# Kernel tuning notes

Measured on AMD Instinct MI355X. Metric: run time of the kernel, lower is better.

The kernel has to match this reference:

```python
import jax, jax.numpy as jnp
import numpy as np

EPS = 1e-8
LN_EPS = 1e-5

def _layernorm(x, g, b):
    mu = jnp.mean(x, axis=-1, keepdims=True)
    var = jnp.mean((x - mu) ** 2, axis=-1, keepdims=True)
    return (x - mu) / jnp.sqrt(var + LN_EPS) * g + b

def setup_inputs() -> dict:
    key = jax.random.key(0)
    ks = jax.random.split(key, 10)
    B, S = 8192, 4096
    input_dim, hidden_dim = 4, 256
    h4 = hidden_dim // 4  # 64
    price_series = jax.random.uniform(ks[0], (B, S, 1), dtype=jnp.float32) + 0.5
    # 4 parallel encoders stacked on leading axis: Linear(input_dim->h4) + LayerNorm(h4)
    enc_w = jax.random.normal(ks[1], (4, input_dim, h4), dtype=jnp.float32) * 0.5
    enc_b = jax.random.normal(ks[2], (4, h4), dtype=jnp.float32) * 0.02
    enc_g = jnp.ones((4, h4), dtype=jnp.float32)
    enc_beta = jnp.zeros((4, h4), dtype=jnp.float32)
    # regime head: Linear(hidden_dim->64) + ReLU + (Dropout eval=identity) + Linear(64->4)
    head_w1 = jax.random.normal(ks[3], (hidden_dim, 64), dtype=jnp.float32) * 0.0625
    head_b1 = jnp.zeros((64,), dtype=jnp.float32)
    head_w2 = jax.random.normal(ks[4], (64, 4), dtype=jnp.float32) * 0.125
    head_b2 = jnp.zeros((4,), dtype=jnp.float32)
    return {"price_series": price_series, "enc_w": enc_w, "enc_b": enc_b,
            "enc_g": enc_g, "enc_beta": enc_beta,
            "head_w1": head_w1, "head_b1": head_b1,
            "head_w2": head_w2, "head_b2": head_b2}

def reference(price_series, enc_w, enc_b, enc_g, enc_beta, head_w1, head_b1, head_w2, head_b2):
    prices = price_series[:, :, 0]  # [B, S]
    B, S = prices.shape
    # Rolling SMA(20) with clamped window start, via cumsum (single pass, no per-step loop)
    csum = jnp.concatenate([jnp.zeros((B, 1), prices.dtype), jnp.cumsum(prices, axis=1)], axis=1)  # [B, S+1]
    i = jnp.arange(S)
    start20 = jnp.maximum(0, i - 19)
    cnt20 = (i - start20 + 1).astype(prices.dtype)
    sma20 = (csum[:, i + 1] - csum[:, start20]) / cnt20  # [B, S]
    trend_signal = (prices - sma20) / (sma20 + EPS)
    f_trend = jnp.mean(trend_signal, axis=1, keepdims=True)  # [B,1]
    # momentum over last 10 steps
    p_last = prices[:, -1:]
    p_m10 = prices[:, -10:-9]
    f_mom = (p_last - p_m10) / (p_m10 + EPS)  # [B,1]
    # mean reversion
    p_mean = jnp.mean(prices, axis=1, keepdims=True)
    f_mr = (p_last - p_mean) / (p_mean + EPS)  # [B,1]
    # cycle: coefficient of variation (torch.std is unbiased, ddof=1)
    f_cyc = jnp.std(prices, axis=1, ddof=1, keepdims=True) / (p_mean + EPS)  # [B,1]
    combined = jnp.concatenate([f_trend, f_mom, f_mr, f_cyc], axis=1)  # [B, 4]
    # 4 parallel encoders: Linear -> ReLU -> LayerNorm
    pre = jnp.einsum('bi,eio->ebo', combined, enc_w) + enc_b[:, None, :]  # [4, B, 64]
    feats = _layernorm(jax.nn.relu(pre), enc_g[:, None, :], enc_beta[:, None, :])  # [4, B, 64]
    # concat order: trend, momentum, mean_rev, cycle along feature dim
    regime_features = jnp.transpose(feats, (1, 0, 2)).reshape(B, -1)  # [B, 256]
    h = jax.nn.relu(regime_features @ head_w1 + head_b1)
    regime_probs = jax.nn.softmax(h @ head_w2 + head_b2, axis=1)  # [B, 4]
    return (regime_features, regime_probs)
```

## Files before the change

kernel.cpp:

```cpp
#include <hip/hip_runtime.h>

#define EPS 1e-8f
#define LN_EPS 1e-5f
#define NROWS 8192
#define SLEN 4096
#define PROBS_OFF 2097152

typedef __attribute__((ext_vector_type(8))) short bf16x8;
typedef __attribute__((ext_vector_type(4))) float f32x4;

__device__ __forceinline__ short f2bf(float f) {
    unsigned u = __float_as_uint(f);
    unsigned r = (u + 0x7FFFu + ((u >> 16) & 1u)) >> 16;
    return (short)r;
}

__global__ __launch_bounds__(256) void k_features(const float* __restrict__ prices,
                                                  float* __restrict__ out) {
    __shared__ float s[SLEN];
    __shared__ float red[12];
    const int b = blockIdx.x;
    const int t = threadIdx.x;
    const float* rowp = prices + (size_t)b * SLEN;

    #pragma unroll
    for (int i = 0; i < 4; ++i) {
        int idx = (i * 256 + t) * 4;
        float4 v = *(const float4*)(rowp + idx);
        *(float4*)(s + idx) = v;
    }
    __syncthreads();

    const int p0 = t * 16;
    float seg[16], prev[20];
    #pragma unroll
    for (int i = 0; i < 4; ++i)
        *(float4*)(seg + 4*i) = *(const float4*)(s + p0 + 4*i);
    #pragma unroll
    for (int i = 0; i < 5; ++i) {
        int base = p0 - 20 + 4*i;
        float4 pv;
        if (base >= 0) pv = *(const float4*)(s + base);
        else pv = make_float4(0.f, 0.f, 0.f, 0.f);
        *(float4*)(prev + 4*i) = pv;
    }

    float W = seg[0];
    #pragma unroll
    for (int j = 1; j < 20; ++j) W += prev[j];

    float x = seg[0];
    float sum = x, sq = x * x;
    float cnt = fminf((float)(p0 + 1), 20.0f);
    float sma = W * __builtin_amdgcn_rcpf(cnt);
    float ts = (x - sma) * __builtin_amdgcn_rcpf(sma + EPS);
    #pragma unroll
    for (int j = 1; j < 16; ++j) {
        x = seg[j];
        W += x - prev[j];
        sum += x;
        sq = fmaf(x, x, sq);
        float c2 = fminf((float)(p0 + j + 1), 20.0f);
        float sm = W * __builtin_amdgcn_rcpf(c2);
        ts += (x - sm) * __builtin_amdgcn_rcpf(sm + EPS);
    }

    #pragma unroll
    for (int off = 32; off > 0; off >>= 1) {
        sum += __shfl_xor(sum, off);
        sq  += __shfl_xor(sq,  off);
        ts  += __shfl_xor(ts,  off);
    }
    const int wv = t >> 6, lane = t & 63;
    if (lane == 0) { red[wv*3] = sum; red[wv*3+1] = sq; red[wv*3+2] = ts; }
    __syncthreads();

    if (t == 0) {
        float S = red[0] + red[3] + red[6] + red[9];
        float Q = red[1] + red[4] + red[7] + red[10];
        float T = red[2] + red[5] + red[8] + red[11];
        float mean = S * (1.0f / 4096.0f);
        float var  = fmaxf((Q - 4096.0f * mean * mean) * (1.0f / 4095.0f), 0.0f);
        float p_last = s[SLEN - 1];
        float p_m10  = s[SLEN - 10];
        float4 c;
        c.x = T * (1.0f / 4096.0f);
        c.y = (p_last - p_m10) / (p_m10 + EPS);
        c.z = (p_last - mean) / (mean + EPS);
        c.w = sqrtf(var) / (mean + EPS);
        *(float4*)(out + (size_t)b * 256) = c;
    }
}

#define ROWS 32

__global__ __launch_bounds__(256) void k_head(
    float* __restrict__ out,
    const float* __restrict__ enc_w, const float* __restrict__ enc_b,
    const float* __restrict__ enc_g, const float* __restrict__ enc_bt,
    const float* __restrict__ w1, const float* __restrict__ b1,
    const float* __restrict__ w2, const float* __restrict__ b2)
{
    __shared__ float comb[ROWS][4];
    __shared__ short rfb[ROWS][264];
    __shared__ float hbuf[ROWS][68];

    const int t = threadIdx.x;
    const int r0 = blockIdx.x * ROWS;
    const int lane = t & 63, wave = t >> 6;
    const int l15 = lane & 15, q = lane >> 4;

    if (t < ROWS * 4)
        comb[t >> 2][t & 3] = out[(size_t)(r0 + (t >> 2)) * 256 + (t & 3)];

    bf16x8 bfrag[8];
    #pragma unroll
    for (int kt = 0; kt < 8; ++kt) {
        #pragma unroll
        for (int j = 0; j < 8; ++j) {
            int k = kt * 32 + q * 8 + j;
            bfrag[kt][j] = f2bf(w1[k * 64 + wave * 16 + l15]);
        }
    }

    const float ew0 = enc_w[wave * 256 + lane];
    const float ew1v = enc_w[wave * 256 + 64 + lane];
    const float ew2v = enc_w[wave * 256 + 128 + lane];
    const float ew3v = enc_w[wave * 256 + 192 + lane];
    const float ebv = enc_b[t], egv = enc_g[t], btv = enc_bt[t];

    __syncthreads();

    for (int r = 0; r < ROWS; ++r) {
        float4 cb = *(const float4*)comb[r];
        float v = fmaf(cb.x, ew0, fmaf(cb.y, ew1v, fmaf(cb.z, ew2v, fmaf(cb.w, ew3v, ebv))));
        v = fmaxf(v, 0.0f);
        float sm = v;
        #pragma unroll
        for (int off = 32; off > 0; off >>= 1) sm += __shfl_xor(sm, off);
        float mu = sm * (1.0f / 64.0f);
        float d = v - mu;
        float vs = d * d;
        #pragma unroll
        for (int off = 32; off > 0; off >>= 1) vs += __shfl_xor(vs, off);
        float y = fmaf(d * rsqrtf(vs * (1.0f / 64.0f) + LN_EPS), egv, btv);
        out[(size_t)(r0 + r) * 256 + t] = y;
        rfb[r][t] = f2bf(y);
    }
    __syncthreads();

    f32x4 acc0 = {0.f, 0.f, 0.f, 0.f}, acc1 = {0.f, 0.f, 0.f, 0.f};
    #pragma unroll
    for (int kt = 0; kt < 8; ++kt) {
        bf16x8 a0 = *(const bf16x8*)&rfb[l15][kt * 32 + q * 8];
        bf16x8 a1 = *(const bf16x8*)&rfb[16 + l15][kt * 32 + q * 8];
        acc0 = __builtin_amdgcn_mfma_f32_16x16x32_bf16(a0, bfrag[kt], acc0, 0, 0, 0);
        acc1 = __builtin_amdgcn_mfma_f32_16x16x32_bf16(a1, bfrag[kt], acc1, 0, 0, 0);
    }

    const int col = wave * 16 + l15;
    const float b1v = b1[col];
    #pragma unroll
    for (int rg = 0; rg < 4; ++rg) {
        hbuf[q * 4 + rg][col]      = fmaxf(acc0[rg] + b1v, 0.0f);
        hbuf[16 + q * 4 + rg][col] = fmaxf(acc1[rg] + b1v, 0.0f);
    }
    __syncthreads();

    if (t < 128) {
        int r = t >> 2, c = t & 3;
        float lg = b2[c];
        #pragma unroll
        for (int j = 0; j < 64; ++j) lg = fmaf(hbuf[r][j], w2[j * 4 + c], lg);
        float mx = fmaxf(lg, __shfl_xor(lg, 1, 4));
        mx = fmaxf(mx, __shfl_xor(mx, 2, 4));
        float ex = __expf(lg - mx);
        float s2 = ex + __shfl_xor(ex, 1, 4);
        s2 += __shfl_xor(s2, 2, 4);
        out[PROBS_OFF + (size_t)(r0 + r) * 4 + c] = ex / s2;
    }
}

extern "C" void kernel_launch(void* const* d_in, const int* in_sizes, int n_in,
                              void* d_out, int out_size, void* d_ws, size_t ws_size,
                              hipStream_t stream) {
    const float* prices  = (const float*)d_in[0];
    const float* enc_w   = (const float*)d_in[1];
    const float* enc_b   = (const float*)d_in[2];
    const float* enc_g   = (const float*)d_in[3];
    const float* enc_bt  = (const float*)d_in[4];
    const float* head_w1 = (const float*)d_in[5];
    const float* head_b1 = (const float*)d_in[6];
    const float* head_w2 = (const float*)d_in[7];
    const float* head_b2 = (const float*)d_in[8];
    float* out = (float*)d_out;

    k_features<<<NROWS, 256, 0, stream>>>(prices, out);
    k_head<<<NROWS / ROWS, 256, 0, stream>>>(out, enc_w, enc_b, enc_g, enc_bt,
                                             head_w1, head_b1, head_w2, head_b2);
}
```

Measured before the change: 223.6 us.

## Fuse feature extraction and regime head into one per-row kernel

Merges the statistics kernel and the encoder/MLP head kernel into a single kernel with one block per row. The head is computed in fp32 FMA loops instead of bf16 MFMA, and the features read prices straight from global memory instead of staging the row in LDS. This removes a launch, the round-trip of the combined features through global memory, and the LDS staging, but every block now rereads the 64 KB head_w1 and does scalar matvec work, which could add cache traffic and ALU time to a kernel that is memory-bound.

```diff
diff --git a/kernel.cpp b/kernel.cpp
--- a/kernel.cpp
+++ b/kernel.cpp
@@ -6,43 +6,36 @@
 #define SLEN 4096
 #define PROBS_OFF 2097152
 
-typedef __attribute__((ext_vector_type(8))) short bf16x8;
-typedef __attribute__((ext_vector_type(4))) float f32x4;
+__global__ __launch_bounds__(256) void k_fused(
+    const float* __restrict__ prices,
+    const float* __restrict__ enc_w, const float* __restrict__ enc_b,
+    const float* __restrict__ enc_g, const float* __restrict__ enc_bt,
+    const float* __restrict__ w1, const float* __restrict__ b1,
+    const float* __restrict__ w2, const float* __restrict__ b2,
+    float* __restrict__ out)
+{
+    __shared__ float red[16];
+    __shared__ float tailv[2];
+    __shared__ float rfl[256];
+    __shared__ float hpart[4][64];
 
-__device__ __forceinline__ short f2bf(float f) {
-    unsigned u = __float_as_uint(f);
-    unsigned r = (u + 0x7FFFu + ((u >> 16) & 1u)) >> 16;
-    return (short)r;
-}
+    const int t = threadIdx.x;
+    const int b = blockIdx.x;
+    const int lane = t & 63, wv = t >> 6;
+    const float* rowp = prices + (size_t)b * SLEN;
+    const int p0 = t * 16;
 
-__global__ __launch_bounds__(256) void k_features(const float* __restrict__ prices,
-                                                  float* __restrict__ out) {
-    __shared__ float s[SLEN];
-    __shared__ float red[12];
-    const int b = blockIdx.x;
-    const int t = threadIdx.x;
-    const float* rowp = prices + (size_t)b * SLEN;
-
-    #pragma unroll
-    for (int i = 0; i < 4; ++i) {
-        int idx = (i * 256 + t) * 4;
-        float4 v = *(const float4*)(rowp + idx);
-        *(float4*)(s + idx) = v;
-    }
-    __syncthreads();
-
-    const int p0 = t * 16;
     float seg[16], prev[20];
     #pragma unroll
     for (int i = 0; i < 4; ++i)
-        *(float4*)(seg + 4*i) = *(const float4*)(s + p0 + 4*i);
+        *(float4*)(seg + 4 * i) = *(const float4*)(rowp + p0 + 4 * i);
     #pragma unroll
     for (int i = 0; i < 5; ++i) {
-        int base = p0 - 20 + 4*i;
+        int base = p0 - 20 + 4 * i;
         float4 pv;
-        if (base >= 0) pv = *(const float4*)(s + base);
+        if (base >= 0) pv = *(const float4*)(rowp + base);
         else pv = make_float4(0.f, 0.f, 0.f, 0.f);
-        *(float4*)(prev + 4*i) = pv;
+        *(float4*)(prev + 4 * i) = pv;
     }
 
     float W = seg[0];
@@ -71,113 +64,71 @@
         sq  += __shfl_xor(sq,  off);
         ts  += __shfl_xor(ts,  off);
     }
-    const int wv = t >> 6, lane = t & 63;
-    if (lane == 0) { red[wv*3] = sum; red[wv*3+1] = sq; red[wv*3+2] = ts; }
+    if (lane == 0) { red[wv * 4] = sum; red[wv * 4 + 1] = sq; red[wv * 4 + 2] = ts; }
+    if (t == 255) { tailv[0] = seg[15]; tailv[1] = seg[6]; }
     __syncthreads();
 
-    if (t == 0) {
-        float S = red[0] + red[3] + red[6] + red[9];
-        float Q = red[1] + red[4] + red[7] + red[10];
-        float T = red[2] + red[5] + red[8] + red[11];
-        float mean = S * (1.0f / 4096.0f);
-        float var  = fmaxf((Q - 4096.0f * mean * mean) * (1.0f / 4095.0f), 0.0f);
-        float p_last = s[SLEN - 1];
-        float p_m10  = s[SLEN - 10];
-        float4 c;
-        c.x = T * (1.0f / 4096.0f);
-        c.y = (p_last - p_m10) / (p_m10 + EPS);
-        c.z = (p_last - mean) / (mean + EPS);
-        c.w = sqrtf(var) / (mean + EPS);
-        *(float4*)(out + (size_t)b * 256) = c;
-    }
-}
+    float S = red[0] + red[4] + red[8]  + red[12];
+    float Q = red[1] + red[5] + red[9]  + red[13];
+    float T = red[2] + red[6] + red[10] + red[14];
+    float mean = S * (1.0f / 4096.0f);
+    float var  = fmaxf((Q - 4096.0f * mean * mean) * (1.0f / 4095.0f), 0.0f);
+    float p_last = tailv[0], p_m10 = tailv[1];
+    float c0 = T * (1.0f / 4096.0f);
+    float c1 = (p_last - p_m10) / (p_m10 + EPS);
+    float c2f = (p_last - mean) / (mean + EPS);
+    float c3 = sqrtf(var) / (mean + EPS);
 
-#define ROWS 32
-
-__global__ __launch_bounds__(256) void k_head(
-    float* __restrict__ out,
-    const float* __restrict__ enc_w, const float* __restrict__ enc_b,
-    const float* __restrict__ enc_g, const float* __restrict__ enc_bt,
-    const float* __restrict__ w1, const float* __restrict__ b1,
-    const float* __restrict__ w2, const float* __restrict__ b2)
-{
-    __shared__ float comb[ROWS][4];
-    __shared__ short rfb[ROWS][264];
-    __shared__ float hbuf[ROWS][68];
-
-    const int t = threadIdx.x;
-    const int r0 = blockIdx.x * ROWS;
-    const int lane = t & 63, wave = t >> 6;
-    const int l15 = lane & 15, q = lane >> 4;
-
-    if (t < ROWS * 4)
-        comb[t >> 2][t & 3] = out[(size_t)(r0 + (t >> 2)) * 256 + (t & 3)];
-
-    bf16x8 bfrag[8];
+    float v = enc_b[t];
+    v = fmaf(c0, enc_w[wv * 256 + lane],       v);
+    v = fmaf(c1, enc_w[wv * 256 + 64 + lane],  v);
+    v = fmaf(c2f, enc_w[wv * 256 + 128 + lane], v);
+    v = fmaf(c3, enc_w[wv * 256 + 192 + lane], v);
+    v = fmaxf(v, 0.0f);
+    float sm = v;
     #pragma unroll
-    for (int kt = 0; kt < 8; ++kt) {
-        #pragma unroll
-        for (int j = 0; j < 8; ++j) {
-            int k = kt * 32 + q * 8 + j;
-            bfrag[kt][j] = f2bf(w1[k * 64 + wave * 16 + l15]);
-        }
-    }
-
-    const float ew0 = enc_w[wave * 256 + lane];
-    const float ew1v = enc_w[wave * 256 + 64 + lane];
-    const float ew2v = enc_w[wave * 256 + 128 + lane];
-    const float ew3v = enc_w[wave * 256 + 192 + lane];
-    const float ebv = enc_b[t], egv = enc_g[t], btv = enc_bt[t];
-
+    for (int off = 32; off > 0; off >>= 1) sm += __shfl_xor(sm, off);
+    float mu = sm * (1.0f / 64.0f);
+    float d = v - mu;
+    float vs = d * d;
+    #pragma unroll
+    for (int off = 32; off > 0; off >>= 1) vs += __shfl_xor(vs, off);
+    float y = fmaf(d * rsqrtf(vs * (1.0f / 64.0f) + LN_EPS), enc_g[t], enc_bt[t]);
+    out[(size_t)b * 256 + t] = y;
+    rfl[t] = y;
     __syncthreads();
 
-    for (int r = 0; r < ROWS; ++r) {
-        float4 cb = *(const float4*)comb[r];
-        float v = fmaf(cb.x, ew0, fmaf(cb.y, ew1v, fmaf(cb.z, ew2v, fmaf(cb.w, ew3v, ebv))));
-        v = fmaxf(v, 0.0f);
-        float sm = v;
-        #pragma unroll
-        for (int off = 32; off > 0; off >>= 1) sm += __shfl_xor(sm, off);
-        float mu = sm * (1.0f / 64.0f);
-        float d = v - mu;
-        float vs = d * d;
-        #pragma unroll
-        for (int off = 32; off > 0; off >>= 1) vs += __shfl_xor(vs, off);
-        float y = fmaf(d * rsqrtf(vs * (1.0f / 64.0f) + LN_EPS), egv, btv);
-        out[(size_t)(r0 + r) * 256 + t] = y;
-        rfb[r][t] = f2bf(y);
+    {
+        float acc = 0.0f;
+        const float* w1p = w1 + (size_t)(wv * 64) * 64 + lane;
+        #pragma unroll 8
+        for (int k = 0; k < 64; ++k)
+            acc = fmaf(rfl[wv * 64 + k], w1p[k * 64], acc);
+        hpart[wv][lane] = acc;
     }
     __syncthreads();
 
-    f32x4 acc0 = {0.f, 0.f, 0.f, 0.f}, acc1 = {0.f, 0.f, 0.f, 0.f};
-    #pragma unroll
-    for (int kt = 0; kt < 8; ++kt) {
-        bf16x8 a0 = *(const bf16x8*)&rfb[l15][kt * 32 + q * 8];
-        bf16x8 a1 = *(const bf16x8*)&rfb[16 + l15][kt * 32 + q * 8];
-        acc0 = __builtin_amdgcn_mfma_f32_16x16x32_bf16(a0, bfrag[kt], acc0, 0, 0, 0);
-        acc1 = __builtin_amdgcn_mfma_f32_16x16x32_bf16(a1, bfrag[kt], acc1, 0, 0, 0);
-    }
-
-    const int col = wave * 16 + l15;
-    const float b1v = b1[col];
-    #pragma unroll
-    for (int rg = 0; rg < 4; ++rg) {
-        hbuf[q * 4 + rg][col]      = fmaxf(acc0[rg] + b1v, 0.0f);
-        hbuf[16 + q * 4 + rg][col] = fmaxf(acc1[rg] + b1v, 0.0f);
-    }
-    __syncthreads();
-
-    if (t < 128) {
-        int r = t >> 2, c = t & 3;
-        float lg = b2[c];
+    if (t < 64) {
+        float h = hpart[0][t] + hpart[1][t] + hpart[2][t] + hpart[3][t] + b1[t];
+        h = fmaxf(h, 0.0f);
+        float4 wrow = *(const float4*)(w2 + t * 4);
+        float l0 = h * wrow.x, l1 = h * wrow.y, l2 = h * wrow.z, l3 = h * wrow.w;
         #pragma unroll
-        for (int j = 0; j < 64; ++j) lg = fmaf(hbuf[r][j], w2[j * 4 + c], lg);
-        float mx = fmaxf(lg, __shfl_xor(lg, 1, 4));
-        mx = fmaxf(mx, __shfl_xor(mx, 2, 4));
-        float ex = __expf(lg - mx);
-        float s2 = ex + __shfl_xor(ex, 1, 4);
-        s2 += __shfl_xor(s2, 2, 4);
-        out[PROBS_OFF + (size_t)(r0 + r) * 4 + c] = ex / s2;
+        for (int off = 32; off > 0; off >>= 1) {
+            l0 += __shfl_xor(l0, off);
+            l1 += __shfl_xor(l1, off);
+            l2 += __shfl_xor(l2, off);
+            l3 += __shfl_xor(l3, off);
+        }
+        if (t == 0) {
+            l0 += b2[0]; l1 += b2[1]; l2 += b2[2]; l3 += b2[3];
+            float mx = fmaxf(fmaxf(l0, l1), fmaxf(l2, l3));
+            float e0 = __expf(l0 - mx), e1 = __expf(l1 - mx);
+            float e2 = __expf(l2 - mx), e3 = __expf(l3 - mx);
+            float inv = 1.0f / (e0 + e1 + e2 + e3);
+            float4 pr = make_float4(e0 * inv, e1 * inv, e2 * inv, e3 * inv);
+            *(float4*)(out + PROBS_OFF + (size_t)b * 4) = pr;
+        }
     }
 }
 
@@ -195,7 +146,6 @@
     const float* head_b2 = (const float*)d_in[8];
     float* out = (float*)d_out;
 
-    k_features<<<NROWS, 256, 0, stream>>>(prices, out);
-    k_head<<<NROWS / ROWS, 256, 0, stream>>>(out, enc_w, enc_b, enc_g, enc_bt,
-                                             head_w1, head_b1, head_w2, head_b2);
+    k_fused<<<NROWS, 256, 0, stream>>>(prices, enc_w, enc_b, enc_g, enc_bt,
+                                       head_w1, head_b1, head_w2, head_b2, out);
 }
```

Result: slower. 228.4 us (+2.1%).

## Process one price row per wavefront with direct global loads, no LDS

Applied to the files above, without the earlier changes.

The feature kernel now gives each 64-lane wavefront a whole row, and each lane handles 64 consecutive elements loaded straight from global memory instead of staging the row in shared memory. The block-level reduction and syncthreads go away, leaving only a wave shuffle reduction. The combined features are written to a workspace buffer rather than the output. Per-lane loads are now strided by 256 bytes across lanes, which hurts coalescing. The register count also grows (a 64-float segment per lane), which may lower occupancy on a memory-bound kernel.

```diff
diff --git a/kernel.cpp b/kernel.cpp
--- a/kernel.cpp
+++ b/kernel.cpp
@@ -15,34 +15,25 @@
     return (short)r;
 }
 
-__global__ __launch_bounds__(256) void k_features(const float* __restrict__ prices,
-                                                  float* __restrict__ out) {
-    __shared__ float s[SLEN];
-    __shared__ float red[12];
-    const int b = blockIdx.x;
+__global__ __launch_bounds__(256) void k_feat(const float* __restrict__ prices,
+                                              float* __restrict__ comb) {
     const int t = threadIdx.x;
+    const int lane = t & 63, wv = t >> 6;
+    const int b = blockIdx.x * 4 + wv;
     const float* rowp = prices + (size_t)b * SLEN;
+    const int p0 = lane * 64;
 
+    float seg[64], prev[20];
     #pragma unroll
-    for (int i = 0; i < 4; ++i) {
-        int idx = (i * 256 + t) * 4;
-        float4 v = *(const float4*)(rowp + idx);
-        *(float4*)(s + idx) = v;
-    }
-    __syncthreads();
-
-    const int p0 = t * 16;
-    float seg[16], prev[20];
-    #pragma unroll
-    for (int i = 0; i < 4; ++i)
-        *(float4*)(seg + 4*i) = *(const float4*)(s + p0 + 4*i);
+    for (int i = 0; i < 16; ++i)
+        *(float4*)(seg + 4 * i) = *(const float4*)(rowp + p0 + 4 * i);
     #pragma unroll
     for (int i = 0; i < 5; ++i) {
-        int base = p0 - 20 + 4*i;
+        int base = p0 - 20 + 4 * i;
         float4 pv;
-        if (base >= 0) pv = *(const float4*)(s + base);
+        if (base >= 0) pv = *(const float4*)(rowp + base);
         else pv = make_float4(0.f, 0.f, 0.f, 0.f);
-        *(float4*)(prev + 4*i) = pv;
+        *(float4*)(prev + 4 * i) = pv;
     }
 
     float W = seg[0];
@@ -55,9 +46,10 @@
     float sma = W * __builtin_amdgcn_rcpf(cnt);
     float ts = (x - sma) * __builtin_amdgcn_rcpf(sma + EPS);
     #pragma unroll
-    for (int j = 1; j < 16; ++j) {
+    for (int j = 1; j < 64; ++j) {
         x = seg[j];
-        W += x - prev[j];
+        float old = (j < 20) ? prev[j] : seg[j - 20];
+        W += x - old;
         sum += x;
         sq = fmaf(x, x, sq);
         float c2 = fminf((float)(p0 + j + 1), 20.0f);
@@ -71,31 +63,25 @@
         sq  += __shfl_xor(sq,  off);
         ts  += __shfl_xor(ts,  off);
     }
-    const int wv = t >> 6, lane = t & 63;
-    if (lane == 0) { red[wv*3] = sum; red[wv*3+1] = sq; red[wv*3+2] = ts; }
-    __syncthreads();
+    float p_last = __shfl(seg[63], 63);
+    float p_m10  = __shfl(seg[54], 63);
 
-    if (t == 0) {
-        float S = red[0] + red[3] + red[6] + red[9];
-        float Q = red[1] + red[4] + red[7] + red[10];
-        float T = red[2] + red[5] + red[8] + red[11];
-        float mean = S * (1.0f / 4096.0f);
-        float var  = fmaxf((Q - 4096.0f * mean * mean) * (1.0f / 4095.0f), 0.0f);
-        float p_last = s[SLEN - 1];
-        float p_m10  = s[SLEN - 10];
+    if (lane == 0) {
+        float mean = sum * (1.0f / 4096.0f);
+        float var  = fmaxf((sq - 4096.0f * mean * mean) * (1.0f / 4095.0f), 0.0f);
         float4 c;
-        c.x = T * (1.0f / 4096.0f);
+        c.x = ts * (1.0f / 4096.0f);
         c.y = (p_last - p_m10) / (p_m10 + EPS);
         c.z = (p_last - mean) / (mean + EPS);
         c.w = sqrtf(var) / (mean + EPS);
-        *(float4*)(out + (size_t)b * 256) = c;
+        *(float4*)(comb + (size_t)b * 4) = c;
     }
 }
 
 #define ROWS 32
 
 __global__ __launch_bounds__(256) void k_head(
-    float* __restrict__ out,
+    const float* __restrict__ combg, float* __restrict__ out,
     const float* __restrict__ enc_w, const float* __restrict__ enc_b,
     const float* __restrict__ enc_g, const float* __restrict__ enc_bt,
     const float* __restrict__ w1, const float* __restrict__ b1,
@@ -111,7 +97,7 @@
     const int l15 = lane & 15, q = lane >> 4;
 
     if (t < ROWS * 4)
-        comb[t >> 2][t & 3] = out[(size_t)(r0 + (t >> 2)) * 256 + (t & 3)];
+        comb[t >> 2][t & 3] = combg[(size_t)(r0 + (t >> 2)) * 4 + (t & 3)];
 
     bf16x8 bfrag[8];
     #pragma unroll
@@ -193,9 +179,10 @@
     const float* head_b1 = (const float*)d_in[6];
     const float* head_w2 = (const float*)d_in[7];
     const float* head_b2 = (const float*)d_in[8];
-    float* out = (float*)d_out;
+    float* out  = (float*)d_out;
+    float* comb = (float*)d_ws;
 
-    k_features<<<NROWS, 256, 0, stream>>>(prices, out);
-    k_head<<<NROWS / ROWS, 256, 0, stream>>>(out, enc_w, enc_b, enc_g, enc_bt,
+    k_feat<<<NROWS / 4, 256, 0, stream>>>(prices, comb);
+    k_head<<<NROWS / ROWS, 256, 0, stream>>>(comb, out, enc_w, enc_b, enc_g, enc_bt,
                                              head_w1, head_b1, head_w2, head_b2);
 }
```

Result: no change. 227.8 us (+1.9%).
